# Optimization experiments

Hardware: AMD Instinct MI355X
Metric: run time of the kernel (lower is better)

The kernel has to match this reference:

```python
import jax, jax.numpy as jnp
import numpy as np

N = 100000   # nodes
E = 400000   # edges
G = 1024     # graphs in batch
IN = 4; H = 128; HD = 4; DH = H // HD; L = 3; ED = 4; FF = 2 * H; JK = H * L
SCALE = 1.0 / np.sqrt(DH).astype(np.float32)


def _ln(x, g, b):
    m = x.mean(-1, keepdims=True)
    v = x.var(-1, keepdims=True)
    return (x - m) / jnp.sqrt(v + 1e-5) * g + b


def setup_inputs() -> dict:
    key = jax.random.key(0)
    ks = jax.random.split(key, 24)
    rn = lambda k, s, sc=0.05: jax.random.normal(k, s, jnp.float32) * sc
    return {
        "x": rn(ks[0], (N, IN), 1.0),
        "edge_index": jax.random.randint(ks[1], (2, E), 0, N),
        "edge_attr": rn(ks[2], (E, ED), 1.0),
        "batch": jnp.sort(jax.random.randint(ks[3], (N,), 0, G)),
        "u": rn(ks[4], (G, 1), 1.0),
        "Win": rn(ks[5], (IN, H)), "b_in": jnp.zeros(H),
        "Wq": rn(ks[6], (L, H, H)), "bq": jnp.zeros((L, H)),
        "Wk": rn(ks[7], (L, H, H)), "bk": jnp.zeros((L, H)),
        "Wv": rn(ks[8], (L, H, H)), "bv": jnp.zeros((L, H)),
        "We": rn(ks[9], (L, ED, H)),
        "Wskip": rn(ks[10], (L, H, H)), "bskip": jnp.zeros((L, H)),
        "ln1_g": jnp.ones((L, H)), "ln1_b": jnp.zeros((L, H)),
        "Wf1": rn(ks[11], (L, H, FF)), "bf1": jnp.zeros((L, FF)),
        "Wf2": rn(ks[12], (L, FF, H)), "bf2": jnp.zeros((L, H)),
        "ln2_g": jnp.ones((L, H)), "ln2_b": jnp.zeros((L, H)),
        "Wg1": rn(ks[13], (JK, H)), "bg1": jnp.zeros(H),
        "Wg2": rn(ks[14], (H, 1)), "bg2": jnp.zeros(1),
        "Wh1": rn(ks[15], (JK + 1, H)), "bh1": jnp.zeros(H),
        "Wh2": rn(ks[16], (H, 3)), "bh2": jnp.zeros(3),
    }


def reference(x, edge_index, edge_attr, batch, u,
              Win, b_in, Wq, bq, Wk, bk, Wv, bv, We, Wskip, bskip,
              ln1_g, ln1_b, Wf1, bf1, Wf2, bf2, ln2_g, ln2_b,
              Wg1, bg1, Wg2, bg2, Wh1, bh1, Wh2, bh2):
    src, dst = edge_index[0], edge_index[1]
    h = x @ Win + b_in                                   # [N,H]
    xs = []
    for l in range(L):
        q = (h @ Wq[l] + bq[l]).reshape(N, HD, DH)
        k_n = h @ Wk[l] + bk[l]
        v_n = h @ Wv[l] + bv[l]
        e = edge_attr @ We[l]                            # [E,H] edge bias
        ke = (k_n[src] + e).reshape(E, HD, DH)
        ve = (v_n[src] + e).reshape(E, HD, DH)
        logits = (q[dst] * ke).sum(-1) * SCALE           # [E,HD]
        m = jax.ops.segment_max(logits, dst, N)
        p = jnp.exp(logits - m[dst])
        s = jax.ops.segment_sum(p, dst, N)
        alpha = p / (s[dst] + 1e-16)                     # segment softmax per dst node
        agg = jax.ops.segment_sum(alpha[:, :, None] * ve, dst, N).reshape(N, H)
        attn = agg + h @ Wskip[l] + bskip[l]             # root weight (skip lin)
        h = _ln(h + attn, ln1_g[l], ln1_b[l])
        ff = jax.nn.relu(h @ Wf1[l] + bf1[l]) @ Wf2[l] + bf2[l]
        h = _ln(h + ff, ln2_g[l], ln2_b[l])
        xs.append(h)
    xc = jnp.concatenate(xs, -1)                         # JumpingKnowledge 'cat' [N,JK]
    gate = (jax.nn.relu(xc @ Wg1 + bg1) @ Wg2 + bg2)[:, 0]  # [N]
    gm = jax.ops.segment_max(gate, batch, G)
    gp = jnp.exp(gate - gm[batch])
    gs = jax.ops.segment_sum(gp, batch, G)
    w = gp / (gs[batch] + 1e-16)                         # per-graph softmax
    pooled = jax.ops.segment_sum(w[:, None] * xc, batch, G)  # [G,JK]
    out = jnp.concatenate([pooled, u], 1)                # [G,JK+1]
    return jax.nn.relu(out @ Wh1 + bh1) @ Wh2 + bh2      # [G,3]
```

## Files before the change

kernel.cpp:

```cpp
#include <hip/hip_runtime.h>
#include <math.h>

#define H 128
#define LAYERS 3
#define FFDIM 256
#define JK 384
#define ATT_SCALE 0.17677669529663687f

typedef unsigned short u16;
typedef __attribute__((ext_vector_type(4))) float f32x4;
typedef __attribute__((ext_vector_type(8))) short short8;
typedef __attribute__((ext_vector_type(8))) unsigned short ushort8v;

static inline int cdiv(int a, int b) { return (a + b - 1) / b; }

static __device__ __forceinline__ float bf2f(u16 u) {
    union { unsigned int i; float f; } v; v.i = ((unsigned int)u) << 16; return v.f;
}
static __device__ __forceinline__ u16 f2bf(float f) {
    union { float f; unsigned int i; } v; v.f = f;
    unsigned int r = v.i + 0x7FFFu + ((v.i >> 16) & 1u);
    return (u16)(r >> 16);
}

__global__ void hist_kernel(const int* __restrict__ ei, int* __restrict__ counts, int E) {
    int e = blockIdx.x * blockDim.x + threadIdx.x;
    if (e >= E) return;
    atomicAdd(&counts[ei[E + e]], 1);
}

__global__ __launch_bounds__(256) void scan1_kernel(const int* __restrict__ counts,
                                                    int* __restrict__ offsets,
                                                    int* __restrict__ bsum, int N) {
    __shared__ int sh[256];
    int t = threadIdx.x;
    int base = blockIdx.x * 1024 + t * 4;
    int v0 = 0, v1 = 0, v2 = 0, v3 = 0;
    if (base + 3 < N) {
        int4 q = *(const int4*)&counts[base];
        v0 = q.x; v1 = q.y; v2 = q.z; v3 = q.w;
    } else {
        if (base < N) v0 = counts[base];
        if (base + 1 < N) v1 = counts[base + 1];
        if (base + 2 < N) v2 = counts[base + 2];
        if (base + 3 < N) v3 = counts[base + 3];
    }
    int ts = v0 + v1 + v2 + v3;
    sh[t] = ts; __syncthreads();
    for (int off = 1; off < 256; off <<= 1) {
        int x = (t >= off) ? sh[t - off] : 0;
        __syncthreads(); sh[t] += x; __syncthreads();
    }
    int excl = sh[t] - ts;
    if (base < N)     offsets[base]     = excl;
    if (base + 1 < N) offsets[base + 1] = excl + v0;
    if (base + 2 < N) offsets[base + 2] = excl + v0 + v1;
    if (base + 3 < N) offsets[base + 3] = excl + v0 + v1 + v2;
    if (t == 255) bsum[blockIdx.x] = sh[255];
}

__global__ __launch_bounds__(128) void scan2_kernel(const int* __restrict__ bsum,
                                                    int* __restrict__ boffs,
                                                    int* __restrict__ offsets, int nb, int N) {
    __shared__ int sh[128];
    int t = threadIdx.x;
    int s = (t < nb) ? bsum[t] : 0;
    sh[t] = s; __syncthreads();
    for (int off = 1; off < 128; off <<= 1) {
        int x = (t >= off) ? sh[t - off] : 0;
        __syncthreads(); sh[t] += x; __syncthreads();
    }
    if (t < nb) boffs[t] = sh[t] - s;
    if (t == 0) offsets[N] = sh[nb - 1];
}

__global__ __launch_bounds__(256) void scan3_kernel(int* __restrict__ offsets,
                                                    const int* __restrict__ boffs, int N) {
    int add = boffs[blockIdx.x];
    int base = blockIdx.x * 1024 + threadIdx.x * 4;
#pragma unroll
    for (int i = 0; i < 4; ++i)
        if (base + i < N) offsets[base + i] += add;
}

__global__ void scatter_kernel(const int* __restrict__ ei, const float* __restrict__ eattr,
                               const int* __restrict__ offsets,
                               int* __restrict__ cursor, int* __restrict__ psrc,
                               float4* __restrict__ pe, int E) {
    int e = blockIdx.x * blockDim.x + threadIdx.x;
    if (e >= E) return;
    int d = ei[E + e];
    int pos = atomicAdd(&cursor[d], 1);
    int o = offsets[d] + pos;
    psrc[o] = ei[e];
    pe[o] = *(const float4*)&eattr[(size_t)e * 4];
}

__global__ __launch_bounds__(256) void dhist_kernel(const int* __restrict__ counts,
                                                    int* __restrict__ dhist, int N) {
    __shared__ int lh[64];
    int t = threadIdx.x;
    if (t < 64) lh[t] = 0;
    __syncthreads();
    int n = blockIdx.x * 256 + t;
    if (n < N) atomicAdd(&lh[min(counts[n], 63)], 1);
    __syncthreads();
    if (t < 64 && lh[t]) atomicAdd(&dhist[t], lh[t]);
}

__global__ __launch_bounds__(64) void dscan_kernel(const int* __restrict__ dhist,
                                                   int* __restrict__ dcur) {
    __shared__ int sh[64];
    int t = threadIdx.x;
    int s = dhist[t];
    sh[t] = s; __syncthreads();
    for (int off = 1; off < 64; off <<= 1) {
        int x = (t >= off) ? sh[t - off] : 0;
        __syncthreads(); sh[t] += x; __syncthreads();
    }
    dcur[t] = sh[t] - s;
}

__global__ __launch_bounds__(256) void dscatter_kernel(const int* __restrict__ counts,
                                                       int* __restrict__ dcur,
                                                       int* __restrict__ nperm, int N) {
    __shared__ int lh[64], lbase[64];
    int t = threadIdx.x;
    if (t < 64) lh[t] = 0;
    __syncthreads();
    int n = blockIdx.x * 256 + t;
    int b = 0, rank = 0;
    if (n < N) {
        b = min(counts[n], 63);
        rank = atomicAdd(&lh[b], 1);
    }
    __syncthreads();
    if (t < 64 && lh[t]) lbase[t] = atomicAdd(&dcur[t], lh[t]);
    __syncthreads();
    if (n < N) nperm[lbase[b] + rank] = n;
}

__global__ void graph_bounds_kernel(const int* __restrict__ batch, int* __restrict__ gstart,
                                    int N, int G) {
    int g = blockIdx.x * blockDim.x + threadIdx.x;
    if (g > G) return;
    int lo = 0, hi = N;
    while (lo < hi) { int mid = (lo + hi) >> 1; if (batch[mid] < g) lo = mid + 1; else hi = mid; }
    gstart[g] = lo;
}

struct TD { const float* src; int dstoff, K, N; };
struct TA { TD d[19]; };

__global__ __launch_bounds__(256) void wconv_kernel(TA a, u16* __restrict__ WT) {
    TD d = a.d[blockIdx.y];
    int i = blockIdx.x * 256 + threadIdx.x;
    int tot = d.K * d.N;
    if (i >= tot) return;
    int c = i / d.K, k = i - c * d.K;
    WT[d.dstoff + i] = f2bf(d.src[(size_t)k * d.N + c]);
}

__global__ __launch_bounds__(256) void input_proj_kernel(const float* __restrict__ x,
                                                         const float* __restrict__ Win,
                                                         const float* __restrict__ b_in,
                                                         u16* __restrict__ h, int ldh, int N) {
    int idx = blockIdx.x * 256 + threadIdx.x;
    int n = idx >> 6, c = (idx & 63) * 2;
    if (n >= N) return;
    float4 xv = *(const float4*)&x[(size_t)n * 4];
    float o0 = b_in[c]     + xv.x * Win[c]     + xv.y * Win[H + c]     + xv.z * Win[2 * H + c]     + xv.w * Win[3 * H + c];
    float o1 = b_in[c + 1] + xv.x * Win[c + 1] + xv.y * Win[H + c + 1] + xv.z * Win[2 * H + c + 1] + xv.w * Win[3 * H + c + 1];
    ushort2 s; s.x = f2bf(o0); s.y = f2bf(o1);
    *(ushort2*)&h[(size_t)n * ldh + c] = s;
}

__device__ __forceinline__ void stage_tile(const u16* __restrict__ g, int ld, int row0,
                                           int nrows, int kt, u16* __restrict__ sm, int t) {
#pragma unroll
    for (int i = 0; i < 4; ++i) {
        int f = i * 256 + t;
        int row = f >> 3, ck = f & 7;
        int n = row0 + row; if (n >= nrows) n = nrows - 1;
        uint4 v = *(const uint4*)(g + (size_t)n * ld + kt + ck * 8);
        int sw = ck ^ (row & 7);
        *(uint4*)(sm + row * 64 + sw * 8) = v;
    }
}

template <int MODE, int NBY>
__global__ __launch_bounds__(256) void gemm_mfma(
    const u16* __restrict__ A, int lda,
    const u16* __restrict__ WT, int K,
    const float* __restrict__ b0, const float* __restrict__ b1,
    const float* __restrict__ b2, const float* __restrict__ b3,
    const u16* __restrict__ resid16,
    u16* __restrict__ obf, u16* __restrict__ obf2, float* __restrict__ of32,
    int nrows)
{
    alignas(16) __shared__ char smemraw[33792];
    u16* Asm = (u16*)smemraw;
    u16* Bsm = (u16*)(smemraw + 16384);
    float* stage = (float*)smemraw;
    int t = threadIdx.x;
    int lane = t & 63, wid = t >> 6;
    int wr = wid >> 1, wc = wid & 1;

    int T = gridDim.x, id = blockIdx.x;
    int qd = T >> 3, rr = T & 7;
    int xcd = id & 7, pos = id >> 3;
    int swz = (xcd < rr ? xcd * (qd + 1) : rr * (qd + 1) + (xcd - rr) * qd) + pos;
    int by = swz & (NBY - 1);
    int row0 = (swz / NBY) * 128;

    const u16* WTb = WT + (size_t)by * 128 * K;

    f32x4 acc[4][4] = {};

    for (int kt = 0; kt < K; kt += 64) {
        stage_tile(A, lda, row0, nrows, kt, Asm, t);
        stage_tile(WTb, K, 0, 128, kt, Bsm, t);
        __syncthreads();
        int g = lane >> 4;
        int l15 = lane & 15;
#pragma unroll
        for (int kk = 0; kk < 2; ++kk) {
            int cb = kk * 4 + g;
            short8 af[4], bf[4];
#pragma unroll
            for (int mi = 0; mi < 4; ++mi) {
                int r = wr * 64 + mi * 16 + l15;
                af[mi] = *(const short8*)(Asm + r * 64 + ((cb ^ (r & 7)) * 8));
            }
#pragma unroll
            for (int nj = 0; nj < 4; ++nj) {
                int c = wc * 64 + nj * 16 + l15;
                bf[nj] = *(const short8*)(Bsm + c * 64 + ((cb ^ (c & 7)) * 8));
            }
#pragma unroll
            for (int mi = 0; mi < 4; ++mi)
#pragma unroll
                for (int nj = 0; nj < 4; ++nj)
                    acc[mi][nj] = __builtin_amdgcn_mfma_f32_16x16x32_bf16(af[mi], bf[nj], acc[mi][nj], 0, 0, 0);
        }
        __syncthreads();
    }

    int g = lane >> 4, l15 = lane & 15;

    if (MODE == 3) {
        float* gsum = (float*)Asm;
        float part[4][4];
#pragma unroll
        for (int mi = 0; mi < 4; ++mi)
#pragma unroll
            for (int r = 0; r < 4; ++r) part[mi][r] = 0.f;
#pragma unroll
        for (int nj = 0; nj < 4; ++nj) {
            int col = wc * 64 + nj * 16 + l15;
            float bb = b0[col];
            float w2 = b1[col];
#pragma unroll
            for (int mi = 0; mi < 4; ++mi)
#pragma unroll
                for (int r = 0; r < 4; ++r) {
                    float v = fmaxf(acc[mi][nj][r] + bb, 0.f);
                    part[mi][r] = fmaf(v, w2, part[mi][r]);
                }
        }
#pragma unroll
        for (int off = 1; off <= 8; off <<= 1)
#pragma unroll
            for (int mi = 0; mi < 4; ++mi)
#pragma unroll
                for (int r = 0; r < 4; ++r) part[mi][r] += __shfl_xor(part[mi][r], off);
        if (wc == 0 && l15 == 0) {
#pragma unroll
            for (int mi = 0; mi < 4; ++mi)
#pragma unroll
                for (int r = 0; r < 4; ++r)
                    gsum[wr * 64 + mi * 16 + g * 4 + r] = part[mi][r];
        }
        __syncthreads();
        if (wc == 1 && l15 == 0) {
            float bg2v = b2[0];
#pragma unroll
            for (int mi = 0; mi < 4; ++mi)
#pragma unroll
                for (int r = 0; r < 4; ++r) {
                    int lr = wr * 64 + mi * 16 + g * 4 + r;
                    int n = row0 + lr;
                    if (n < nrows) of32[n] = part[mi][r] + gsum[lr] + bg2v;
                }
        }
        return;
    }

    const float* bias;
    u16* ob = nullptr; int ldob = 384;
    if (MODE == 0) {
        bias = (by == 0) ? b0 : (by == 1) ? b1 : (by == 2) ? b2 : b3;
        if (by < 3) ob = obf + by * 128;
        else { ob = obf2; ldob = 128; }
    } else if (MODE == 1) {
        bias = b0 + by * 128;
        ob = obf + by * 128;
    } else {
        bias = b0;
        ob = obf;
    }

#pragma unroll
    for (int p = 0; p < 2; ++p) {
        if (wr == p) {
#pragma unroll
            for (int nj = 0; nj < 4; ++nj) {
                int col = wc * 64 + nj * 16 + l15;
                float bb = bias[col];
#pragma unroll
                for (int mi = 0; mi < 4; ++mi)
#pragma unroll
                    for (int r = 0; r < 4; ++r) {
                        float v = acc[mi][nj][r] + bb;
                        if (MODE == 1) v = fmaxf(v, 0.f);
                        stage[(mi * 16 + g * 4 + r) * 132 + col] = v;
                    }
            }
        }
        __syncthreads();
        if (MODE == 2) {
            int sub2 = t & 15, rowg = t >> 4;
#pragma unroll
            for (int it = 0; it < 4; ++it) {
                int lr = it * 16 + rowg;
                int gr = row0 + p * 64 + lr;
                bool ok = gr < nrows;
                int c8 = sub2 * 8;
                float tv[8]; float sum = 0.f, sq = 0.f;
                if (ok) {
                    ushort8v rv = *(const ushort8v*)&resid16[(size_t)gr * 384 + c8];
#pragma unroll
                    for (int i = 0; i < 8; ++i) {
                        tv[i] = stage[lr * 132 + c8 + i] + bf2f(rv[i]);
                        sum += tv[i]; sq += tv[i] * tv[i];
                    }
                }
#pragma unroll
                for (int off = 1; off <= 8; off <<= 1) { sum += __shfl_xor(sum, off); sq += __shfl_xor(sq, off); }
                if (ok) {
                    float mean = sum * (1.f / 128.f);
                    float var = sq * (1.f / 128.f) - mean * mean;
                    float rstd = rsqrtf(var + 1e-5f);
                    ushort8v o;
#pragma unroll
                    for (int i = 0; i < 8; ++i)
                        o[i] = f2bf((tv[i] - mean) * rstd * b1[c8 + i] + b2[c8 + i]);
                    *(ushort8v*)&ob[(size_t)gr * 384 + c8] = o;
                }
            }
        } else {
#pragma unroll
            for (int it = 0; it < 4; ++it) {
                int lr = it * 16 + (t >> 4);
                int gr = row0 + p * 64 + lr;
                if (gr < nrows) {
                    int c8 = l15 * 8;
                    ushort8v o;
#pragma unroll
                    for (int i = 0; i < 8; ++i) o[i] = f2bf(stage[lr * 132 + c8 + i]);
                    *(ushort8v*)&ob[(size_t)gr * ldob + c8] = o;
                }
            }
        }
        __syncthreads();
    }
}

__global__ __launch_bounds__(256) void attn_kernel(
    u16* __restrict__ qkv,
    const u16* __restrict__ h_in, int ld_h,
    const u16* __restrict__ skipb,
    const int* __restrict__ offsets,
    const int* __restrict__ nperm,
    const int* __restrict__ psrc, const float4* __restrict__ pe,
    const float* __restrict__ We_l,
    const float* __restrict__ g1, const float* __restrict__ b1,
    int N)
{
    int tid = threadIdx.x;
    int grp = tid >> 4;
    int sub = tid & 15;
    int idx = blockIdx.x * 16 + grp;
    if (idx >= N) return;
    int n = nperm[idx];
    int d0 = sub * 8;

    float we[4][8];
#pragma unroll
    for (int aa = 0; aa < 4; ++aa) {
        float4 w0 = *(const float4*)&We_l[aa * H + d0];
        float4 w1 = *(const float4*)&We_l[aa * H + d0 + 4];
        we[aa][0] = w0.x; we[aa][1] = w0.y; we[aa][2] = w0.z; we[aa][3] = w0.w;
        we[aa][4] = w1.x; we[aa][5] = w1.y; we[aa][6] = w1.z; we[aa][7] = w1.w;
    }

    ushort8v qraw = *(const ushort8v*)&qkv[(size_t)n * JK + d0];
    float qf[8];
#pragma unroll
    for (int i = 0; i < 8; ++i) qf[i] = bf2f(qraw[i]);

    float qe[4];
#pragma unroll
    for (int aa = 0; aa < 4; ++aa) {
        float s = 0.f;
#pragma unroll
        for (int i = 0; i < 8; ++i) s = fmaf(qf[i], we[aa][i], s);
        s += __shfl_xor(s, 1);
        s += __shfl_xor(s, 2);
        qe[aa] = s;
    }

    float m = -INFINITY, ssum = 0.f;
    float a[8] = {0.f, 0.f, 0.f, 0.f, 0.f, 0.f, 0.f, 0.f};
    float ws0 = 0.f, ws1 = 0.f, ws2 = 0.f, ws3 = 0.f;
    int e0 = offsets[n], e1 = offsets[n + 1];
    if (e0 < e1) {
        int s0i = psrc[e0];
        float4 ea = pe[e0];
        const u16* sr = qkv + (size_t)s0i * JK;
        ushort8v kr = *(const ushort8v*)&sr[H + d0];
        ushort8v vr = *(const ushort8v*)&sr[2 * H + d0];
        for (int j = e0; j < e1; ++j) {
            float4 ea2; ushort8v kr2, vr2;
            if (j + 1 < e1) {
                int s2 = psrc[j + 1];
                ea2 = pe[j + 1];
                const u16* sr2 = qkv + (size_t)s2 * JK;
                kr2 = *(const ushort8v*)&sr2[H + d0];
                vr2 = *(const ushort8v*)&sr2[2 * H + d0];
            }
            float part = 0.f;
#pragma unroll
            for (int i = 0; i < 8; ++i) part = fmaf(qf[i], bf2f(kr[i]), part);
            part += __shfl_xor(part, 1);
            part += __shfl_xor(part, 2);
            float logit = (part + ea.x * qe[0] + ea.y * qe[1] + ea.z * qe[2] + ea.w * qe[3]) * ATT_SCALE;
            float mn = fmaxf(m, logit);
            float corr = __expf(m - mn);
            float p = __expf(logit - mn);
            ssum = ssum * corr + p;
#pragma unroll
            for (int i = 0; i < 8; ++i) a[i] = a[i] * corr + p * bf2f(vr[i]);
            ws0 = ws0 * corr + p * ea.x;
            ws1 = ws1 * corr + p * ea.y;
            ws2 = ws2 * corr + p * ea.z;
            ws3 = ws3 * corr + p * ea.w;
            m = mn;
            kr = kr2; vr = vr2; ea = ea2;
        }
    }
    float inv = 1.f / (ssum + 1e-16f);
#pragma unroll
    for (int i = 0; i < 8; ++i)
        a[i] += ws0 * we[0][i] + ws1 * we[1][i] + ws2 * we[2][i] + ws3 * we[3][i];

    ushort8v hraw = *(const ushort8v*)&h_in[(size_t)n * ld_h + d0];
    ushort8v skraw = *(const ushort8v*)&skipb[(size_t)n * H + d0];
    float tv[8], sum = 0.f, sq = 0.f;
#pragma unroll
    for (int i = 0; i < 8; ++i) {
        tv[i] = bf2f(hraw[i]) + a[i] * inv + bf2f(skraw[i]);
        sum += tv[i]; sq += tv[i] * tv[i];
    }
#pragma unroll
    for (int off = 1; off <= 8; off <<= 1) { sum += __shfl_xor(sum, off); sq += __shfl_xor(sq, off); }
    float mean = sum * (1.f / 128.f);
    float var = sq * (1.f / 128.f) - mean * mean;
    float rstd = rsqrtf(var + 1e-5f);
    float4 ga = *(const float4*)&g1[d0];
    float4 gb = *(const float4*)&g1[d0 + 4];
    float4 ba = *(const float4*)&b1[d0];
    float4 bb = *(const float4*)&b1[d0 + 4];
    float gg[8] = {ga.x, ga.y, ga.z, ga.w, gb.x, gb.y, gb.z, gb.w};
    float bbv[8] = {ba.x, ba.y, ba.z, ba.w, bb.x, bb.y, bb.z, bb.w};
    ushort8v obv;
#pragma unroll
    for (int i = 0; i < 8; ++i)
        obv[i] = f2bf((tv[i] - mean) * rstd * gg[i] + bbv[i]);
    *(ushort8v*)&qkv[(size_t)n * JK + d0] = obv;
}

#define PCH 512
__global__ __launch_bounds__(256) void pool_kernel(const float* __restrict__ gate,
                                                   const u16* __restrict__ xc,
                                                   const int* __restrict__ gstart,
                                                   const float* __restrict__ u,
                                                   float* __restrict__ pooled, int G) {
    int g = blockIdx.x;
    int t = threadIdx.x;
    int s0 = gstart[g], s1 = gstart[g + 1];
    __shared__ float red[256];
    __shared__ float w[PCH];
    float mx = -INFINITY;
    for (int i = s0 + t; i < s1; i += 256) mx = fmaxf(mx, gate[i]);
    red[t] = mx; __syncthreads();
    for (int off = 128; off; off >>= 1) { if (t < off) red[t] = fmaxf(red[t], red[t + off]); __syncthreads(); }
    float gm = red[0]; __syncthreads();
    float sm = 0.f;
    for (int i = s0 + t; i < s1; i += 256) sm += __expf(gate[i] - gm);
    red[t] = sm; __syncthreads();
    for (int off = 128; off; off >>= 1) { if (t < off) red[t] += red[t + off]; __syncthreads(); }
    float inv = 1.f / (red[0] + 1e-16f);
    float acc0 = 0.f, acc1 = 0.f;
    for (int base = s0; base < s1; base += PCH) {
        int cnt = min(PCH, s1 - base);
        __syncthreads();
        for (int i = t; i < cnt; i += 256) w[i] = __expf(gate[base + i] - gm) * inv;
        __syncthreads();
        for (int c = 0; c < cnt; ++c) {
            const u16* row = xc + (size_t)(base + c) * JK;
            float wc = w[c];
            acc0 = fmaf(wc, bf2f(row[t]), acc0);
            if (t < 128) acc1 = fmaf(wc, bf2f(row[t + 256]), acc1);
        }
    }
    pooled[(size_t)g * (JK + 1) + t] = acc0;
    if (t < 128) pooled[(size_t)g * (JK + 1) + t + 256] = acc1;
    if (t == 0) pooled[(size_t)g * (JK + 1) + JK] = u[g];
}

__global__ __launch_bounds__(128) void head_kernel(const float* __restrict__ pooled,
                                                   const float* __restrict__ Wh1,
                                                   const float* __restrict__ bh1,
                                                   const float* __restrict__ Wh2,
                                                   const float* __restrict__ bh2,
                                                   float* __restrict__ out, int G) {
    int g = blockIdx.x;
    int j = threadIdx.x;
    __shared__ float hid[128];
    float acc = bh1[j];
    const float* pr = pooled + (size_t)g * (JK + 1);
    for (int k = 0; k < JK + 1; ++k) acc = fmaf(pr[k], Wh1[(size_t)k * H + j], acc);
    hid[j] = fmaxf(acc, 0.f);
    __syncthreads();
    if (j < 3) {
        float o = bh2[j];
        for (int k = 0; k < H; ++k) o += hid[k] * Wh2[k * 3 + j];
        out[(size_t)g * 3 + j] = o;
    }
}

extern "C" void kernel_launch(void* const* d_in, const int* in_sizes, int n_in,
                              void* d_out, int out_size, void* d_ws, size_t ws_size,
                              hipStream_t stream) {
    const float* x     = (const float*)d_in[0];
    const int*   ei    = (const int*)d_in[1];
    const float* eattr = (const float*)d_in[2];
    const int*   batch = (const int*)d_in[3];
    const float* u     = (const float*)d_in[4];
    const float* Win   = (const float*)d_in[5];
    const float* b_in  = (const float*)d_in[6];
    const float* Wq    = (const float*)d_in[7];
    const float* bq    = (const float*)d_in[8];
    const float* Wk    = (const float*)d_in[9];
    const float* bk    = (const float*)d_in[10];
    const float* Wv    = (const float*)d_in[11];
    const float* bv    = (const float*)d_in[12];
    const float* We    = (const float*)d_in[13];
    const float* Wskip = (const float*)d_in[14];
    const float* bskip = (const float*)d_in[15];
    const float* ln1_g = (const float*)d_in[16];
    const float* ln1_b = (const float*)d_in[17];
    const float* Wf1   = (const float*)d_in[18];
    const float* bf1   = (const float*)d_in[19];
    const float* Wf2   = (const float*)d_in[20];
    const float* bf2   = (const float*)d_in[21];
    const float* ln2_g = (const float*)d_in[22];
    const float* ln2_b = (const float*)d_in[23];
    const float* Wg1   = (const float*)d_in[24];
    const float* bg1   = (const float*)d_in[25];
    const float* Wg2   = (const float*)d_in[26];
    const float* bg2   = (const float*)d_in[27];
    const float* Wh1   = (const float*)d_in[28];
    const float* bh1   = (const float*)d_in[29];
    const float* Wh2   = (const float*)d_in[30];
    const float* bh2   = (const float*)d_in[31];

    const int N = in_sizes[3];
    const int E = in_sizes[1] / 2;
    const int G = in_sizes[4];

    char* p = (char*)d_ws;
    auto alloc = [&](size_t bytes) { char* r = p; p += (bytes + 255) & ~(size_t)255; return r; };
    int*    counts  = (int*)alloc((size_t)N * 4);
    int*    cursor  = (int*)alloc((size_t)N * 4);
    int*    offsets = (int*)alloc((size_t)(N + 1) * 4);
    int*    psrc    = (int*)alloc((size_t)E * 4);
    float4* pe      = (float4*)alloc((size_t)E * 16);
    int*    nperm   = (int*)alloc((size_t)N * 4);
    int*    gstart  = (int*)alloc((size_t)(G + 1) * 4);
    int*    bsum    = (int*)alloc(128 * 4);
    int*    boffs   = (int*)alloc(128 * 4);
    int*    dhist   = (int*)alloc(64 * 4);
    int*    dcur    = (int*)alloc(64 * 4);
    float*  gate    = (float*)alloc((size_t)N * 4);
    float*  pooled  = (float*)alloc((size_t)G * (JK + 1) * 4);
    u16*    WT      = (u16*)alloc((size_t)442368 * 2);
    u16*    skipb   = (u16*)alloc((size_t)N * H * 2);
    u16*    xc      = (u16*)alloc((size_t)N * JK * 2);
    u16*    qkv     = (u16*)alloc((size_t)N * JK * 2);

    const int QKVS_OFF = 0;
    const int F1_OFF   = 3 * 65536;
    const int F2_OFF   = F1_OFF + 3 * 32768;
    const int G1_OFF   = F2_OFF + 3 * 32768;

    hipMemsetAsync(counts, 0, (size_t)N * 4, stream);
    hipMemsetAsync(cursor, 0, (size_t)N * 4, stream);
    hipMemsetAsync(dhist, 0, 64 * 4, stream);

    int eb = cdiv(E, 256);
    int nb = cdiv(N, 1024);
    int nthb = cdiv(N, 256);
    hist_kernel<<<eb, 256, 0, stream>>>(ei, counts, E);
    scan1_kernel<<<nb, 256, 0, stream>>>(counts, offsets, bsum, N);
    scan2_kernel<<<1, 128, 0, stream>>>(bsum, boffs, offsets, nb, N);
    scan3_kernel<<<nb, 256, 0, stream>>>(offsets, boffs, N);
    scatter_kernel<<<eb, 256, 0, stream>>>(ei, eattr, offsets, cursor, psrc, pe, E);
    dhist_kernel<<<nthb, 256, 0, stream>>>(counts, dhist, N);
    dscan_kernel<<<1, 64, 0, stream>>>(dhist, dcur);
    dscatter_kernel<<<nthb, 256, 0, stream>>>(counts, dcur, nperm, N);
    graph_bounds_kernel<<<cdiv(G + 1, 256), 256, 0, stream>>>(batch, gstart, N, G);

    TA ta;
    for (int l = 0; l < 3; ++l) {
        ta.d[l * 4 + 0] = { Wq    + (size_t)l * 16384, QKVS_OFF + l * 65536 + 0,     128, 128 };
        ta.d[l * 4 + 1] = { Wk    + (size_t)l * 16384, QKVS_OFF + l * 65536 + 16384, 128, 128 };
        ta.d[l * 4 + 2] = { Wv    + (size_t)l * 16384, QKVS_OFF + l * 65536 + 32768, 128, 128 };
        ta.d[l * 4 + 3] = { Wskip + (size_t)l * 16384, QKVS_OFF + l * 65536 + 49152, 128, 128 };
        ta.d[12 + l]    = { Wf1   + (size_t)l * 32768, F1_OFF   + l * 32768,         128, 256 };
        ta.d[15 + l]    = { Wf2   + (size_t)l * 32768, F2_OFF   + l * 32768,         256, 128 };
    }
    ta.d[18] = { Wg1, G1_OFF, 384, 128 };
    dim3 wg(cdiv(49152, 256), 19);
    wconv_kernel<<<wg, 256, 0, stream>>>(ta, WT);

    input_proj_kernel<<<cdiv(N * 64, 256), 256, 0, stream>>>(x, Win, b_in, xc, JK, N);

    int gb = cdiv(N, 128);
    int nb16 = cdiv(N, 16);
    for (int l = 0; l < LAYERS; ++l) {
        const u16* hin = xc + (size_t)((l == 0) ? 0 : (l - 1) * H);
        gemm_mfma<0, 4><<<gb * 4, 256, 0, stream>>>(
            hin, JK, WT + QKVS_OFF + (size_t)l * 65536, 128,
            bq + l * H, bk + l * H, bv + l * H, bskip + l * H,
            nullptr, qkv, skipb, nullptr, N);
        attn_kernel<<<nb16, 256, 0, stream>>>(qkv, hin, JK, skipb, offsets, nperm, psrc, pe,
                                              We + (size_t)l * 4 * H, ln1_g + l * H, ln1_b + l * H,
                                              N);
        gemm_mfma<1, 2><<<gb * 2, 256, 0, stream>>>(
            qkv, JK, WT + F1_OFF + (size_t)l * 32768, 128,
            bf1 + (size_t)l * FFDIM, nullptr, nullptr, nullptr,
            nullptr, qkv + H, nullptr, nullptr, N);
        gemm_mfma<2, 1><<<gb, 256, 0, stream>>>(
            qkv + H, JK, WT + F2_OFF + (size_t)l * 32768, 256,
            bf2 + (size_t)l * H, ln2_g + (size_t)l * H, ln2_b + (size_t)l * H, nullptr,
            qkv, xc + (size_t)l * H, nullptr, nullptr, N);
    }

    gemm_mfma<3, 1><<<gb, 256, 0, stream>>>(
        xc, JK, WT + G1_OFF, JK,
        bg1, Wg2, bg2, nullptr,
        nullptr, nullptr, nullptr, gate, N);
    pool_kernel<<<G, 256, 0, stream>>>(gate, xc, gstart, u, pooled, G);
    head_kernel<<<G, 128, 0, stream>>>(pooled, Wh1, bh1, Wh2, bh2, (float*)d_out, G);
}
```

Measured before the change: 647.4 us.

## Process edges in pairs with dual online-softmax states and fold residual into skip GEMM

The attention kernel now walks each node's incoming edges two at a time, keeping two independent online-softmax accumulators that are merged at the end. This doubles the gathers in flight and breaks the serial dependency chain of the per-edge softmax update. Separately, the skip-projection GEMM epilogue now adds the input h into the skip output, so the attention kernel no longer reads h. The cost is higher register pressure from the duplicated accumulators, plus an extra tail path for odd degrees.

```diff
diff --git a/kernel.cpp b/kernel.cpp
--- a/kernel.cpp
+++ b/kernel.cpp
@@ -364,10 +364,16 @@
                 int lr = it * 16 + (t >> 4);
                 int gr = row0 + p * 64 + lr;
                 if (gr < nrows) {
-                    int c8 = l15 * 8;
+                    int c8 = (t & 15) * 8;
                     ushort8v o;
-#pragma unroll
-                    for (int i = 0; i < 8; ++i) o[i] = f2bf(stage[lr * 132 + c8 + i]);
+                    if (MODE == 0 && by == 3) {
+                        ushort8v hv = *(const ushort8v*)&A[(size_t)gr * lda + c8];
+#pragma unroll
+                        for (int i = 0; i < 8; ++i) o[i] = f2bf(stage[lr * 132 + c8 + i] + bf2f(hv[i]));
+                    } else {
+#pragma unroll
+                        for (int i = 0; i < 8; ++i) o[i] = f2bf(stage[lr * 132 + c8 + i]);
+                    }
                     *(ushort8v*)&ob[(size_t)gr * ldob + c8] = o;
                 }
             }
@@ -378,7 +384,6 @@
 
 __global__ __launch_bounds__(256) void attn_kernel(
     u16* __restrict__ qkv,
-    const u16* __restrict__ h_in, int ld_h,
     const u16* __restrict__ skipb,
     const int* __restrict__ offsets,
     const int* __restrict__ nperm,
@@ -420,56 +425,110 @@
         qe[aa] = s;
     }
 
-    float m = -INFINITY, ssum = 0.f;
-    float a[8] = {0.f, 0.f, 0.f, 0.f, 0.f, 0.f, 0.f, 0.f};
-    float ws0 = 0.f, ws1 = 0.f, ws2 = 0.f, ws3 = 0.f;
-    int e0 = offsets[n], e1 = offsets[n + 1];
-    if (e0 < e1) {
-        int s0i = psrc[e0];
-        float4 ea = pe[e0];
-        const u16* sr = qkv + (size_t)s0i * JK;
+    float m0 = -INFINITY, ss0 = 0.f, m1 = -INFINITY, ss1 = 0.f;
+    float a0[8] = {}, a1[8] = {};
+    float w0a = 0.f, w0b = 0.f, w0c = 0.f, w0d = 0.f;
+    float w1a = 0.f, w1b = 0.f, w1c = 0.f, w1d = 0.f;
+    int e0v = offsets[n], e1v = offsets[n + 1];
+    int deg = e1v - e0v;
+    int npairs = deg >> 1;
+
+    if (npairs > 0) {
+        int j0 = e0v;
+        int sA = psrc[j0], sB = psrc[j0 + 1];
+        float4 eaA = pe[j0], eaB = pe[j0 + 1];
+        const u16* srA = qkv + (size_t)sA * JK;
+        const u16* srB = qkv + (size_t)sB * JK;
+        ushort8v krA = *(const ushort8v*)&srA[H + d0];
+        ushort8v vrA = *(const ushort8v*)&srA[2 * H + d0];
+        ushort8v krB = *(const ushort8v*)&srB[H + d0];
+        ushort8v vrB = *(const ushort8v*)&srB[2 * H + d0];
+        for (int it = 0; it < npairs; ++it) {
+            float4 eaA2, eaB2; ushort8v krA2, vrA2, krB2, vrB2;
+            if (it + 1 < npairs) {
+                int jn = e0v + (it + 1) * 2;
+                int sA2 = psrc[jn], sB2 = psrc[jn + 1];
+                eaA2 = pe[jn]; eaB2 = pe[jn + 1];
+                const u16* srA2 = qkv + (size_t)sA2 * JK;
+                const u16* srB2 = qkv + (size_t)sB2 * JK;
+                krA2 = *(const ushort8v*)&srA2[H + d0];
+                vrA2 = *(const ushort8v*)&srA2[2 * H + d0];
+                krB2 = *(const ushort8v*)&srB2[H + d0];
+                vrB2 = *(const ushort8v*)&srB2[2 * H + d0];
+            }
+            float pA = 0.f, pB = 0.f;
+#pragma unroll
+            for (int i = 0; i < 8; ++i) {
+                pA = fmaf(qf[i], bf2f(krA[i]), pA);
+                pB = fmaf(qf[i], bf2f(krB[i]), pB);
+            }
+            pA += __shfl_xor(pA, 1); pB += __shfl_xor(pB, 1);
+            pA += __shfl_xor(pA, 2); pB += __shfl_xor(pB, 2);
+            float lgA = (pA + eaA.x * qe[0] + eaA.y * qe[1] + eaA.z * qe[2] + eaA.w * qe[3]) * ATT_SCALE;
+            float lgB = (pB + eaB.x * qe[0] + eaB.y * qe[1] + eaB.z * qe[2] + eaB.w * qe[3]) * ATT_SCALE;
+            float mnA = fmaxf(m0, lgA);
+            float mnB = fmaxf(m1, lgB);
+            float cA = __expf(m0 - mnA), cB = __expf(m1 - mnB);
+            float pvA = __expf(lgA - mnA), pvB = __expf(lgB - mnB);
+            ss0 = ss0 * cA + pvA;
+            ss1 = ss1 * cB + pvB;
+#pragma unroll
+            for (int i = 0; i < 8; ++i) {
+                a0[i] = a0[i] * cA + pvA * bf2f(vrA[i]);
+                a1[i] = a1[i] * cB + pvB * bf2f(vrB[i]);
+            }
+            w0a = w0a * cA + pvA * eaA.x; w0b = w0b * cA + pvA * eaA.y;
+            w0c = w0c * cA + pvA * eaA.z; w0d = w0d * cA + pvA * eaA.w;
+            w1a = w1a * cB + pvB * eaB.x; w1b = w1b * cB + pvB * eaB.y;
+            w1c = w1c * cB + pvB * eaB.z; w1d = w1d * cB + pvB * eaB.w;
+            m0 = mnA; m1 = mnB;
+            krA = krA2; vrA = vrA2; eaA = eaA2;
+            krB = krB2; vrB = vrB2; eaB = eaB2;
+        }
+    }
+    if (deg & 1) {
+        int j = e1v - 1;
+        int s = psrc[j];
+        float4 ea = pe[j];
+        const u16* sr = qkv + (size_t)s * JK;
         ushort8v kr = *(const ushort8v*)&sr[H + d0];
         ushort8v vr = *(const ushort8v*)&sr[2 * H + d0];
-        for (int j = e0; j < e1; ++j) {
-            float4 ea2; ushort8v kr2, vr2;
-            if (j + 1 < e1) {
-                int s2 = psrc[j + 1];
-                ea2 = pe[j + 1];
-                const u16* sr2 = qkv + (size_t)s2 * JK;
-                kr2 = *(const ushort8v*)&sr2[H + d0];
-                vr2 = *(const ushort8v*)&sr2[2 * H + d0];
-            }
-            float part = 0.f;
-#pragma unroll
-            for (int i = 0; i < 8; ++i) part = fmaf(qf[i], bf2f(kr[i]), part);
-            part += __shfl_xor(part, 1);
-            part += __shfl_xor(part, 2);
-            float logit = (part + ea.x * qe[0] + ea.y * qe[1] + ea.z * qe[2] + ea.w * qe[3]) * ATT_SCALE;
-            float mn = fmaxf(m, logit);
-            float corr = __expf(m - mn);
-            float p = __expf(logit - mn);
-            ssum = ssum * corr + p;
-#pragma unroll
-            for (int i = 0; i < 8; ++i) a[i] = a[i] * corr + p * bf2f(vr[i]);
-            ws0 = ws0 * corr + p * ea.x;
-            ws1 = ws1 * corr + p * ea.y;
-            ws2 = ws2 * corr + p * ea.z;
-            ws3 = ws3 * corr + p * ea.w;
-            m = mn;
-            kr = kr2; vr = vr2; ea = ea2;
-        }
-    }
-    float inv = 1.f / (ssum + 1e-16f);
+        float part = 0.f;
+#pragma unroll
+        for (int i = 0; i < 8; ++i) part = fmaf(qf[i], bf2f(kr[i]), part);
+        part += __shfl_xor(part, 1);
+        part += __shfl_xor(part, 2);
+        float lg = (part + ea.x * qe[0] + ea.y * qe[1] + ea.z * qe[2] + ea.w * qe[3]) * ATT_SCALE;
+        float mn = fmaxf(m0, lg);
+        float c = __expf(m0 - mn);
+        float pv = __expf(lg - mn);
+        ss0 = ss0 * c + pv;
+#pragma unroll
+        for (int i = 0; i < 8; ++i) a0[i] = a0[i] * c + pv * bf2f(vr[i]);
+        w0a = w0a * c + pv * ea.x; w0b = w0b * c + pv * ea.y;
+        w0c = w0c * c + pv * ea.z; w0d = w0d * c + pv * ea.w;
+        m0 = mn;
+    }
+    float mm = fmaxf(m0, m1);
+    if (mm > -INFINITY) {
+        float c0 = (m0 > -INFINITY) ? __expf(m0 - mm) : 0.f;
+        float c1 = (m1 > -INFINITY) ? __expf(m1 - mm) : 0.f;
+        ss0 = ss0 * c0 + ss1 * c1;
+#pragma unroll
+        for (int i = 0; i < 8; ++i) a0[i] = a0[i] * c0 + a1[i] * c1;
+        w0a = w0a * c0 + w1a * c1; w0b = w0b * c0 + w1b * c1;
+        w0c = w0c * c0 + w1c * c1; w0d = w0d * c0 + w1d * c1;
+    }
+    float inv = 1.f / (ss0 + 1e-16f);
 #pragma unroll
     for (int i = 0; i < 8; ++i)
-        a[i] += ws0 * we[0][i] + ws1 * we[1][i] + ws2 * we[2][i] + ws3 * we[3][i];
-
-    ushort8v hraw = *(const ushort8v*)&h_in[(size_t)n * ld_h + d0];
+        a0[i] += w0a * we[0][i] + w0b * we[1][i] + w0c * we[2][i] + w0d * we[3][i];
+
     ushort8v skraw = *(const ushort8v*)&skipb[(size_t)n * H + d0];
     float tv[8], sum = 0.f, sq = 0.f;
 #pragma unroll
     for (int i = 0; i < 8; ++i) {
-        tv[i] = bf2f(hraw[i]) + a[i] * inv + bf2f(skraw[i]);
+        tv[i] = a0[i] * inv + bf2f(skraw[i]);
         sum += tv[i]; sq += tv[i] * tv[i];
     }
 #pragma unroll
@@ -655,7 +714,7 @@
             hin, JK, WT + QKVS_OFF + (size_t)l * 65536, 128,
             bq + l * H, bk + l * H, bv + l * H, bskip + l * H,
             nullptr, qkv, skipb, nullptr, N);
-        attn_kernel<<<nb16, 256, 0, stream>>>(qkv, hin, JK, skipb, offsets, nperm, psrc, pe,
+        attn_kernel<<<nb16, 256, 0, stream>>>(qkv, skipb, offsets, nperm, psrc, pe,
                                               We + (size_t)l * 4 * H, ln1_g + l * H, ln1_b + l * H,
                                               N);
         gemm_mfma<1, 2><<<gb * 2, 256, 0, stream>>>(
```

Measured after the change: 660.5 us. +2.0%, slower.
